# Kernel optimization log

Hardware: AMD Instinct MI355X
Metric: run time of the kernel (lower is better)

## Reference

```python
import jax, jax.numpy as jnp
import numpy as np

N = 100_000          # nodes
E = 1_600_000        # edges (avg degree 16)
IN_DIM = 128
POS_DIM = 16
CONTENT_DIM = IN_DIM - POS_DIM   # 112
H = 4                # num_heads
D = 32               # out_dim per head (H*D == IN_DIM -> identity residual)
D4 = D // 4          # pos feature dim per head


def setup_inputs() -> dict:
    key = jax.random.key(0)
    ks = jax.random.split(key, 10)
    feat = jax.random.normal(ks[0], (N, IN_DIM), jnp.float32)
    src = jax.random.randint(ks[1], (E,), 0, N, jnp.int32)
    dst = jax.random.randint(ks[2], (E,), 0, N, jnp.int32)
    # learned parameters (xavier-ish scale)
    Wc = jax.random.normal(ks[3], (H * D, CONTENT_DIM), jnp.float32) * (1.0 / np.sqrt(CONTENT_DIM))
    Wp = jax.random.normal(ks[4], (H * D4, POS_DIM), jnp.float32) * (1.0 / np.sqrt(POS_DIM))
    attn_src = jax.random.normal(ks[5], (1, H, D), jnp.float32) * 0.1
    attn_dst = jax.random.normal(ks[6], (1, H, D), jnp.float32) * 0.1
    pos_attn_src = jax.random.normal(ks[7], (1, H, D4), jnp.float32) * 0.1
    pos_attn_dst = jax.random.normal(ks[8], (1, H, D4), jnp.float32) * 0.1
    att_comb = jnp.full((H, 2), 0.5, jnp.float32)  # nn.init.constant_(0.5)
    return {"feat": feat, "src": src, "dst": dst, "Wc": Wc, "Wp": Wp,
            "attn_src": attn_src, "attn_dst": attn_dst,
            "pos_attn_src": pos_attn_src, "pos_attn_dst": pos_attn_dst,
            "att_comb": att_comb}


def reference(feat, src, dst, Wc, Wp, attn_src, attn_dst,
              pos_attn_src, pos_attn_dst, att_comb):
    content = feat[:, :-POS_DIM]                       # [N, CONTENT_DIM]
    pos = feat[:, -POS_DIM:]                           # [N, POS_DIM]
    hc = (content @ Wc.T).reshape(N, H, D)             # [N, H, D]
    hp = (pos @ Wp.T).reshape(N, H, D4)                # [N, H, D4]

    # per-node attention projections (reduce over feature dim once)
    es = jnp.einsum('nhd,hd->nh', hc, attn_src[0])     # [N, H]
    ed = jnp.einsum('nhd,hd->nh', hc, attn_dst[0])
    ps = jnp.einsum('nhd,hd->nh', hp, pos_attn_src[0])
    pd = jnp.einsum('nhd,hd->nh', hp, pos_attn_dst[0])

    # per-edge combined score + leaky relu (slope 0.2)
    content_e = es[src] + ed[dst]                      # [E, H]
    pos_e = ps[src] + pd[dst]
    e = content_e * att_comb[:, 0] + pos_e * att_comb[:, 1]
    e = jnp.where(e > 0, e, 0.2 * e)

    # edge softmax grouped by destination node
    emax = jax.ops.segment_max(e, dst, num_segments=N)     # [N, H]
    ex = jnp.exp(e - emax[dst])
    esum = jax.ops.segment_sum(ex, dst, num_segments=N)    # [N, H]
    a = ex / esum[dst]                                     # [E, H]

    # weighted message aggregation: ft[v] = sum_{(u,v)} a_uv * hc[u]
    ft = jax.ops.segment_sum(a[:, :, None] * hc[src], dst, num_segments=N)  # [N, H, D]

    h = ft.reshape(N, H * D) + feat   # identity residual (in_dim == out_dim*num_heads)
    diversity_loss = jnp.zeros((), jnp.float32)  # eval path
    return h, diversity_loss
```

## Files before the change

### kernel.cpp

```cpp
#include <hip/hip_runtime.h>
#include <hip/hip_bf16.h>

#define NN 100000
#define NE 1600000
#define FD 128
#define CD 112
#define PDIM 16
#define NH 4
#define NB_SCAN 391
#define NSHARD 8
#define SHARD 12500
#define NE4 400000
#define NB_E4 1563
#define NB_HIST (NSHARD * NB_E4)

#define NOUT 144
#define MBLK 64
#define NGB 1563

#define GRP 72
#define NGRP 196
#define FUSE_GRID (NGRP * GRP)

using bf16x8 = __attribute__((ext_vector_type(8))) short;
using f32x4  = __attribute__((ext_vector_type(4))) float;

__device__ __forceinline__ unsigned short f2bf(float x) {
    union { float f; unsigned int u; } v; v.f = x;
    return (unsigned short)((v.u + 0x7fffu + ((v.u >> 16) & 1u)) >> 16);
}
__device__ __forceinline__ float bf_lo(unsigned int u) { return __uint_as_float(u << 16); }
__device__ __forceinline__ float bf_hi(unsigned int u) { return __uint_as_float(u & 0xffff0000u); }

__device__ __forceinline__ bf16x8 pack8(const float4 g0, const float4 g1) {
    bf16x8 r;
    r[0] = (short)f2bf(g0.x); r[1] = (short)f2bf(g0.y);
    r[2] = (short)f2bf(g0.z); r[3] = (short)f2bf(g0.w);
    r[4] = (short)f2bf(g1.x); r[5] = (short)f2bf(g1.y);
    r[6] = (short)f2bf(g1.z); r[7] = (short)f2bf(g1.w);
    return r;
}

__global__ __launch_bounds__(256) void hist_prep_kernel(
    const int* __restrict__ dst, int* __restrict__ deg,
    const float* __restrict__ Wc, const float* __restrict__ Wp,
    const float* __restrict__ attn_src, const float* __restrict__ attn_dst,
    const float* __restrict__ pos_attn_src, const float* __restrict__ pos_attn_dst,
    const float* __restrict__ att_comb, unsigned short* __restrict__ wt)
{
    __shared__ float sA[NH * FD], sB[NH * FD];
    const int t = threadIdx.x;
    if (blockIdx.x < NB_HIST) {
        const int shard = blockIdx.x & (NSHARD - 1);
        const int i4 = (blockIdx.x >> 3) * 256 + t;
        if (i4 >= NE4) return;
        const int4 d4 = ((const int4*)dst)[i4];
        const int lo = shard * SHARD, hi = lo + SHARD;
        if (d4.x >= lo && d4.x < hi) atomicAdd(&deg[d4.x], 1);
        if (d4.y >= lo && d4.y < hi) atomicAdd(&deg[d4.y], 1);
        if (d4.z >= lo && d4.z < hi) atomicAdd(&deg[d4.z], 1);
        if (d4.w >= lo && d4.w < hi) atomicAdd(&deg[d4.w], 1);
        return;
    }
    #pragma unroll
    for (int r = 0; r < 2; ++r) {
        const int idx = t + r * 256;
        const int h = idx >> 7, k = idx & 127;
        const float c0 = att_comb[h * 2], c1 = att_comb[h * 2 + 1];
        float sa = 0.f, sb = 0.f;
        if (k < CD) {
            #pragma unroll 8
            for (int d = 0; d < 32; ++d) {
                const float wv = Wc[(size_t)(h * 32 + d) * CD + k];
                sa = fmaf(wv, attn_src[h * 32 + d], sa);
                sb = fmaf(wv, attn_dst[h * 32 + d], sb);
            }
            sa *= c0; sb *= c0;
        } else {
            const int k2 = k - CD;
            #pragma unroll
            for (int d4 = 0; d4 < 8; ++d4) {
                const float wv = Wp[(h * 8 + d4) * PDIM + k2];
                sa = fmaf(wv, pos_attn_src[h * 8 + d4], sa);
                sb = fmaf(wv, pos_attn_dst[h * 8 + d4], sb);
            }
            sa *= c1; sb *= c1;
        }
        sA[idx] = sa; sB[idx] = sb;
    }
    __syncthreads();
    #pragma unroll
    for (int it = 0; it < 72; ++it) {
        const int e = t + it * 256;
        const int row = e >> 7, k = e & 127;
        float val;
        if (row < 128)      val = (k < CD) ? Wc[(size_t)row * CD + k] : 0.f;
        else if (row < 132) val = sA[(row - 128) * FD + k];
        else if (row < 136) val = sB[(row - 132) * FD + k];
        else                val = 0.f;
        wt[e] = f2bf(val);
    }
}

__global__ __launch_bounds__(256) void scan1_kernel(const int* __restrict__ deg,
                                                    int* __restrict__ tmp,
                                                    int* __restrict__ bsum) {
    __shared__ int sh[256];
    const int t = threadIdx.x, b = blockIdx.x, i = b * 256 + t;
    const int v = (i < NN) ? deg[i] : 0;
    sh[t] = v;
    __syncthreads();
    #pragma unroll
    for (int off = 1; off < 256; off <<= 1) {
        const int x = (t >= off) ? sh[t - off] : 0;
        __syncthreads();
        sh[t] += x;
        __syncthreads();
    }
    if (i < NN) tmp[i] = sh[t] - v;
    if (t == 255) bsum[b] = sh[t];
}

__global__ __launch_bounds__(512) void scan2_kernel(int* __restrict__ bsum) {
    __shared__ int sh[512];
    const int t = threadIdx.x;
    const int v = (t < NB_SCAN) ? bsum[t] : 0;
    sh[t] = v;
    __syncthreads();
    #pragma unroll
    for (int off = 1; off < 512; off <<= 1) {
        const int x = (t >= off) ? sh[t - off] : 0;
        __syncthreads();
        sh[t] += x;
        __syncthreads();
    }
    if (t < NB_SCAN) bsum[t] = sh[t] - v;
}

__global__ __launch_bounds__(256) void scan3_kernel(const int* __restrict__ tmp,
                                                    const int* __restrict__ bsum,
                                                    int* __restrict__ row_ptr,
                                                    int* __restrict__ cursor) {
    const int i = blockIdx.x * 256 + threadIdx.x;
    if (i < NN) {
        const int v = tmp[i] + bsum[blockIdx.x];
        row_ptr[i] = v;
        cursor[i] = v;
    }
    if (i == 0) row_ptr[NN] = NE;
}

__global__ __launch_bounds__(256) void scatter_mfma_kernel(
    const int* __restrict__ src, const int* __restrict__ dst,
    int* __restrict__ cursor, int* __restrict__ col,
    const float* __restrict__ feat, const unsigned short* __restrict__ wt,
    unsigned short* __restrict__ hc_bf, float* __restrict__ A,
    float* __restrict__ B)
{
    const int bid = blockIdx.x;
    const int grp = bid / GRP, r = bid % GRP;
    const int t = threadIdx.x;

    if (r < 64) {
        const int sid = grp * 64 + r;
        const int shard = sid & (NSHARD - 1);
        const int i4 = (sid >> 3) * 256 + t;
        if (i4 >= NE4) return;
        const int4 d4 = ((const int4*)dst)[i4];
        const int4 s4 = ((const int4*)src)[i4];
        const int lo = shard * SHARD, hi = lo + SHARD;
        if (d4.x >= lo && d4.x < hi) col[atomicAdd(&cursor[d4.x], 1)] = s4.x;
        if (d4.y >= lo && d4.y < hi) col[atomicAdd(&cursor[d4.y], 1)] = s4.y;
        if (d4.z >= lo && d4.z < hi) col[atomicAdd(&cursor[d4.z], 1)] = s4.z;
        if (d4.w >= lo && d4.w < hi) col[atomicAdd(&cursor[d4.w], 1)] = s4.w;
        return;
    }

    const int g = grp * 8 + (r - 64);
    if (g >= NGB) return;
    const int n0 = g * MBLK;
    const int w = t >> 6;
    const int lane = t & 63;
    const int mr = lane & 15, quad = lane >> 4;
    const int node_row = n0 + w * 16 + mr;
    const size_t frow = (size_t)(node_row < NN ? node_row : 0) * FD;

    f32x4 acc[9];
    #pragma unroll
    for (int i = 0; i < 9; ++i) acc[i] = (f32x4){0.f, 0.f, 0.f, 0.f};

    #pragma unroll
    for (int kk = 0; kk < 4; ++kk) {
        const float4* fp = (const float4*)(feat + frow + kk * 32 + quad * 8);
        const bf16x8 a = pack8(fp[0], fp[1]);
        #pragma unroll
        for (int tt = 0; tt < 9; ++tt) {
            const bf16x8 b =
                *(const bf16x8*)&wt[(size_t)(tt * 16 + mr) * FD + kk * 32 + quad * 8];
            acc[tt] = __builtin_amdgcn_mfma_f32_16x16x32_bf16(a, b, acc[tt], 0, 0, 0);
        }
    }

    #pragma unroll
    for (int tt = 0; tt < 8; ++tt) {
        const int colc = tt * 16 + mr;
        #pragma unroll
        for (int rr = 0; rr < 4; ++rr) {
            const int node = n0 + w * 16 + quad * 4 + rr;
            if (node < NN) hc_bf[(size_t)node * FD + colc] = f2bf(acc[tt][rr]);
        }
    }
    #pragma unroll
    for (int rr = 0; rr < 4; ++rr) {
        const int node = n0 + w * 16 + quad * 4 + rr;
        if (node < NN) {
            if (mr < 4)      A[(size_t)node * NH + mr] = acc[8][rr];
            else if (mr < 8) B[(size_t)node * NH + (mr - 4)] = acc[8][rr];
        }
    }
}

__global__ __launch_bounds__(256) void agg_kernel(
    const int* __restrict__ row_ptr, const int* __restrict__ col,
    const float* __restrict__ A, const float* __restrict__ B,
    const uint2* __restrict__ hc_u2,
    const float* __restrict__ feat, float* __restrict__ out)
{
    const int n = blockIdx.x * 8 + (threadIdx.x >> 5);
    const int il = threadIdx.x & 31;
    const int hme = il >> 3;
    const int hbase = threadIdx.x & 0x20;
    const int gbase = hbase | (il & 0x18);
    const int r0 = row_ptr[n], r1 = row_ptr[n + 1];
    const float bh = B[(size_t)n * NH + hme];

    float ssum = 0.f;
    float acc0 = 0.f, acc1 = 0.f, acc2 = 0.f, acc3 = 0.f;

    int p = r0;
    while (p < r1) {
        const int cnt = (r1 - p < 32) ? (r1 - p) : 32;
        const int cidx = (il < cnt) ? col[p + il] : 0;
        for (int q = 0; q < cnt; q += 16) {
            const int j = il & 7;
            const int myc0 = __shfl(cidx, hbase | (q + j));
            const int myc1 = __shfl(cidx, hbase | (q + 8 + j));
            float w0 = 0.f, w1 = 0.f;
            if (q + j < cnt) {
                float e = A[(size_t)myc0 * NH + hme] + bh;
                e = e > 0.f ? e : 0.2f * e;
                w0 = __expf(e);
            }
            if (q + 8 + j < cnt) {
                float e = A[(size_t)myc1 * NH + hme] + bh;
                e = e > 0.f ? e : 0.2f * e;
                w1 = __expf(e);
            }
            int cm[16];
            #pragma unroll
            for (int m = 0; m < 16; ++m)
                cm[m] = __shfl(cidx, hbase | (q + m));
            uint2 u[16];
            #pragma unroll
            for (int m = 0; m < 16; ++m)
                u[m] = hc_u2[(size_t)cm[m] * 32 + il];
            #pragma unroll
            for (int m = 0; m < 16; ++m) {
                const float wm = (m < 8) ? __shfl(w0, gbase | m)
                                         : __shfl(w1, gbase | (m - 8));
                ssum += wm;
                acc0 = fmaf(wm, bf_lo(u[m].x), acc0);
                acc1 = fmaf(wm, bf_hi(u[m].x), acc1);
                acc2 = fmaf(wm, bf_lo(u[m].y), acc2);
                acc3 = fmaf(wm, bf_hi(u[m].y), acc3);
            }
        }
        p += cnt;
    }

    const float inv = ssum > 0.f ? 1.f / ssum : 0.f;
    const float4 fv = ((const float4*)(feat + (size_t)n * FD))[il];
    float4 ov;
    ov.x = acc0 * inv + fv.x;
    ov.y = acc1 * inv + fv.y;
    ov.z = acc2 * inv + fv.z;
    ov.w = acc3 * inv + fv.w;
    ((float4*)(out + (size_t)n * FD))[il] = ov;

    if (blockIdx.x == 0 && threadIdx.x == 0) out[(size_t)NN * FD] = 0.f;
}

extern "C" void kernel_launch(void* const* d_in, const int* in_sizes, int n_in,
                              void* d_out, int out_size, void* d_ws, size_t ws_size,
                              hipStream_t stream) {
    const float* feat         = (const float*)d_in[0];
    const int*   src          = (const int*)d_in[1];
    const int*   dst          = (const int*)d_in[2];
    const float* Wc           = (const float*)d_in[3];
    const float* Wp           = (const float*)d_in[4];
    const float* attn_src     = (const float*)d_in[5];
    const float* attn_dst     = (const float*)d_in[6];
    const float* pos_attn_src = (const float*)d_in[7];
    const float* pos_attn_dst = (const float*)d_in[8];
    const float* att_comb     = (const float*)d_in[9];
    float* out = (float*)d_out;

    char* w = (char*)d_ws;
    unsigned short* hc_bf = (unsigned short*)w;        w += (size_t)NN * FD * 2;
    float* A       = (float*)w;                        w += (size_t)NN * NH * 4;
    float* B       = (float*)w;                        w += (size_t)NN * NH * 4;
    int*   deg     = (int*)w;                          w += (size_t)NN * 4;
    int*   tmp     = (int*)w;                          w += (size_t)NN * 4;
    int*   row_ptr = (int*)w;                          w += (size_t)(NN + 4) * 4;
    int*   cursor  = (int*)w;                          w += (size_t)NN * 4;
    int*   bsum    = (int*)w;                          w += 512 * 4;
    unsigned short* wt = (unsigned short*)w;           w += (size_t)NOUT * FD * 2;
    int*   col     = (int*)w;

    hipMemsetAsync(deg, 0, (size_t)NN * sizeof(int), stream);
    hist_prep_kernel<<<NB_HIST + 1, 256, 0, stream>>>(dst, deg, Wc, Wp,
        attn_src, attn_dst, pos_attn_src, pos_attn_dst, att_comb, wt);
    scan1_kernel<<<NB_SCAN, 256, 0, stream>>>(deg, tmp, bsum);
    scan2_kernel<<<1, 512, 0, stream>>>(bsum);
    scan3_kernel<<<NB_SCAN, 256, 0, stream>>>(tmp, bsum, row_ptr, cursor);
    scatter_mfma_kernel<<<FUSE_GRID, 256, 0, stream>>>(src, dst, cursor, col,
        feat, wt, hc_bf, A, B);
    agg_kernel<<<NN / 8, 256, 0, stream>>>(row_ptr, col, A, B,
                                           (const uint2*)hc_bf, feat, out);
}
```

Measured before the change: 362.8 us.

## Record per-edge rank during histogram to make CSR scatter atomic-free

```diff
diff --git a/kernel.cpp b/kernel.cpp
--- a/kernel.cpp
+++ b/kernel.cpp
@@ -12,7 +12,6 @@
 #define SHARD 12500
 #define NE4 400000
 #define NB_E4 1563
-#define NB_HIST (NSHARD * NB_E4)
 
 #define NOUT 144
 #define MBLK 64
@@ -41,8 +40,7 @@
     return r;
 }
 
-__global__ __launch_bounds__(256) void hist_prep_kernel(
-    const int* __restrict__ dst, int* __restrict__ deg,
+__global__ __launch_bounds__(256) void prep_kernel(
     const float* __restrict__ Wc, const float* __restrict__ Wp,
     const float* __restrict__ attn_src, const float* __restrict__ attn_dst,
     const float* __restrict__ pos_attn_src, const float* __restrict__ pos_attn_dst,
@@ -50,18 +48,6 @@
 {
     __shared__ float sA[NH * FD], sB[NH * FD];
     const int t = threadIdx.x;
-    if (blockIdx.x < NB_HIST) {
-        const int shard = blockIdx.x & (NSHARD - 1);
-        const int i4 = (blockIdx.x >> 3) * 256 + t;
-        if (i4 >= NE4) return;
-        const int4 d4 = ((const int4*)dst)[i4];
-        const int lo = shard * SHARD, hi = lo + SHARD;
-        if (d4.x >= lo && d4.x < hi) atomicAdd(&deg[d4.x], 1);
-        if (d4.y >= lo && d4.y < hi) atomicAdd(&deg[d4.y], 1);
-        if (d4.z >= lo && d4.z < hi) atomicAdd(&deg[d4.z], 1);
-        if (d4.w >= lo && d4.w < hi) atomicAdd(&deg[d4.w], 1);
-        return;
-    }
     #pragma unroll
     for (int r = 0; r < 2; ++r) {
         const int idx = t + r * 256;
@@ -102,6 +88,76 @@
     }
 }
 
+__global__ __launch_bounds__(256) void hist_mfma_kernel(
+    const int* __restrict__ dst, int* __restrict__ deg,
+    unsigned char* __restrict__ rank_b,
+    const float* __restrict__ feat, const unsigned short* __restrict__ wt,
+    unsigned short* __restrict__ hc_bf, float* __restrict__ A,
+    float* __restrict__ B)
+{
+    const int bid = blockIdx.x;
+    const int grp = bid / GRP, r = bid % GRP;
+    const int t = threadIdx.x;
+
+    if (r < 64) {
+        const int sid = grp * 64 + r;
+        const int shard = sid & (NSHARD - 1);
+        const int i4 = (sid >> 3) * 256 + t;
+        if (i4 >= NE4) return;
+        const int4 d4 = ((const int4*)dst)[i4];
+        const int lo = shard * SHARD, hi = lo + SHARD;
+        const int e0 = i4 * 4;
+        if (d4.x >= lo && d4.x < hi) rank_b[e0 + 0] = (unsigned char)atomicAdd(&deg[d4.x], 1);
+        if (d4.y >= lo && d4.y < hi) rank_b[e0 + 1] = (unsigned char)atomicAdd(&deg[d4.y], 1);
+        if (d4.z >= lo && d4.z < hi) rank_b[e0 + 2] = (unsigned char)atomicAdd(&deg[d4.z], 1);
+        if (d4.w >= lo && d4.w < hi) rank_b[e0 + 3] = (unsigned char)atomicAdd(&deg[d4.w], 1);
+        return;
+    }
+
+    const int g = grp * 8 + (r - 64);
+    if (g >= NGB) return;
+    const int n0 = g * MBLK;
+    const int w = t >> 6;
+    const int lane = t & 63;
+    const int mr = lane & 15, quad = lane >> 4;
+    const int node_row = n0 + w * 16 + mr;
+    const size_t frow = (size_t)(node_row < NN ? node_row : 0) * FD;
+
+    f32x4 acc[9];
+    #pragma unroll
+    for (int i = 0; i < 9; ++i) acc[i] = (f32x4){0.f, 0.f, 0.f, 0.f};
+
+    #pragma unroll
+    for (int kk = 0; kk < 4; ++kk) {
+        const float4* fp = (const float4*)(feat + frow + kk * 32 + quad * 8);
+        const bf16x8 a = pack8(fp[0], fp[1]);
+        #pragma unroll
+        for (int tt = 0; tt < 9; ++tt) {
+            const bf16x8 b =
+                *(const bf16x8*)&wt[(size_t)(tt * 16 + mr) * FD + kk * 32 + quad * 8];
+            acc[tt] = __builtin_amdgcn_mfma_f32_16x16x32_bf16(a, b, acc[tt], 0, 0, 0);
+        }
+    }
+
+    #pragma unroll
+    for (int tt = 0; tt < 8; ++tt) {
+        const int colc = tt * 16 + mr;
+        #pragma unroll
+        for (int rr = 0; rr < 4; ++rr) {
+            const int node = n0 + w * 16 + quad * 4 + rr;
+            if (node < NN) hc_bf[(size_t)node * FD + colc] = f2bf(acc[tt][rr]);
+        }
+    }
+    #pragma unroll
+    for (int rr = 0; rr < 4; ++rr) {
+        const int node = n0 + w * 16 + quad * 4 + rr;
+        if (node < NN) {
+            if (mr < 4)      A[(size_t)node * NH + mr] = acc[8][rr];
+            else if (mr < 8) B[(size_t)node * NH + (mr - 4)] = acc[8][rr];
+        }
+    }
+}
+
 __global__ __launch_bounds__(256) void scan1_kernel(const int* __restrict__ deg,
                                                     int* __restrict__ tmp,
                                                     int* __restrict__ bsum) {
@@ -139,85 +195,26 @@
 
 __global__ __launch_bounds__(256) void scan3_kernel(const int* __restrict__ tmp,
                                                     const int* __restrict__ bsum,
-                                                    int* __restrict__ row_ptr,
-                                                    int* __restrict__ cursor) {
+                                                    int* __restrict__ row_ptr) {
     const int i = blockIdx.x * 256 + threadIdx.x;
-    if (i < NN) {
-        const int v = tmp[i] + bsum[blockIdx.x];
-        row_ptr[i] = v;
-        cursor[i] = v;
-    }
+    if (i < NN) row_ptr[i] = tmp[i] + bsum[blockIdx.x];
     if (i == 0) row_ptr[NN] = NE;
 }
 
-__global__ __launch_bounds__(256) void scatter_mfma_kernel(
+__global__ __launch_bounds__(256) void scatter_kernel(
     const int* __restrict__ src, const int* __restrict__ dst,
-    int* __restrict__ cursor, int* __restrict__ col,
-    const float* __restrict__ feat, const unsigned short* __restrict__ wt,
-    unsigned short* __restrict__ hc_bf, float* __restrict__ A,
-    float* __restrict__ B)
+    const unsigned char* __restrict__ rank_b, const int* __restrict__ row_ptr,
+    int* __restrict__ col)
 {
-    const int bid = blockIdx.x;
-    const int grp = bid / GRP, r = bid % GRP;
-    const int t = threadIdx.x;
-
-    if (r < 64) {
-        const int sid = grp * 64 + r;
-        const int shard = sid & (NSHARD - 1);
-        const int i4 = (sid >> 3) * 256 + t;
-        if (i4 >= NE4) return;
-        const int4 d4 = ((const int4*)dst)[i4];
-        const int4 s4 = ((const int4*)src)[i4];
-        const int lo = shard * SHARD, hi = lo + SHARD;
-        if (d4.x >= lo && d4.x < hi) col[atomicAdd(&cursor[d4.x], 1)] = s4.x;
-        if (d4.y >= lo && d4.y < hi) col[atomicAdd(&cursor[d4.y], 1)] = s4.y;
-        if (d4.z >= lo && d4.z < hi) col[atomicAdd(&cursor[d4.z], 1)] = s4.z;
-        if (d4.w >= lo && d4.w < hi) col[atomicAdd(&cursor[d4.w], 1)] = s4.w;
-        return;
-    }
-
-    const int g = grp * 8 + (r - 64);
-    if (g >= NGB) return;
-    const int n0 = g * MBLK;
-    const int w = t >> 6;
-    const int lane = t & 63;
-    const int mr = lane & 15, quad = lane >> 4;
-    const int node_row = n0 + w * 16 + mr;
-    const size_t frow = (size_t)(node_row < NN ? node_row : 0) * FD;
-
-    f32x4 acc[9];
-    #pragma unroll
-    for (int i = 0; i < 9; ++i) acc[i] = (f32x4){0.f, 0.f, 0.f, 0.f};
-
-    #pragma unroll
-    for (int kk = 0; kk < 4; ++kk) {
-        const float4* fp = (const float4*)(feat + frow + kk * 32 + quad * 8);
-        const bf16x8 a = pack8(fp[0], fp[1]);
-        #pragma unroll
-        for (int tt = 0; tt < 9; ++tt) {
-            const bf16x8 b =
-                *(const bf16x8*)&wt[(size_t)(tt * 16 + mr) * FD + kk * 32 + quad * 8];
-            acc[tt] = __builtin_amdgcn_mfma_f32_16x16x32_bf16(a, b, acc[tt], 0, 0, 0);
-        }
-    }
-
-    #pragma unroll
-    for (int tt = 0; tt < 8; ++tt) {
-        const int colc = tt * 16 + mr;
-        #pragma unroll
-        for (int rr = 0; rr < 4; ++rr) {
-            const int node = n0 + w * 16 + quad * 4 + rr;
-            if (node < NN) hc_bf[(size_t)node * FD + colc] = f2bf(acc[tt][rr]);
-        }
-    }
-    #pragma unroll
-    for (int rr = 0; rr < 4; ++rr) {
-        const int node = n0 + w * 16 + quad * 4 + rr;
-        if (node < NN) {
-            if (mr < 4)      A[(size_t)node * NH + mr] = acc[8][rr];
-            else if (mr < 8) B[(size_t)node * NH + (mr - 4)] = acc[8][rr];
-        }
-    }
+    const int i4 = blockIdx.x * 256 + threadIdx.x;
+    if (i4 >= NE4) return;
+    const int4 d4 = ((const int4*)dst)[i4];
+    const int4 s4 = ((const int4*)src)[i4];
+    const unsigned int r4 = ((const unsigned int*)rank_b)[i4];
+    col[row_ptr[d4.x] + (int)(r4 & 0xffu)]         = s4.x;
+    col[row_ptr[d4.y] + (int)((r4 >> 8) & 0xffu)]  = s4.y;
+    col[row_ptr[d4.z] + (int)((r4 >> 16) & 0xffu)] = s4.z;
+    col[row_ptr[d4.w] + (int)(r4 >> 24)]           = s4.w;
 }
 
 __global__ __launch_bounds__(256) void agg_kernel(
@@ -312,19 +309,20 @@
     int*   deg     = (int*)w;                          w += (size_t)NN * 4;
     int*   tmp     = (int*)w;                          w += (size_t)NN * 4;
     int*   row_ptr = (int*)w;                          w += (size_t)(NN + 4) * 4;
-    int*   cursor  = (int*)w;                          w += (size_t)NN * 4;
     int*   bsum    = (int*)w;                          w += 512 * 4;
     unsigned short* wt = (unsigned short*)w;           w += (size_t)NOUT * FD * 2;
-    int*   col     = (int*)w;
+    int*   col     = (int*)w;                          w += (size_t)NE * 4;
+    unsigned char* rank_b = (unsigned char*)w;
 
     hipMemsetAsync(deg, 0, (size_t)NN * sizeof(int), stream);
-    hist_prep_kernel<<<NB_HIST + 1, 256, 0, stream>>>(dst, deg, Wc, Wp,
-        attn_src, attn_dst, pos_attn_src, pos_attn_dst, att_comb, wt);
+    prep_kernel<<<1, 256, 0, stream>>>(Wc, Wp, attn_src, attn_dst,
+                                       pos_attn_src, pos_attn_dst, att_comb, wt);
+    hist_mfma_kernel<<<FUSE_GRID, 256, 0, stream>>>(dst, deg, rank_b,
+                                                    feat, wt, hc_bf, A, B);
     scan1_kernel<<<NB_SCAN, 256, 0, stream>>>(deg, tmp, bsum);
     scan2_kernel<<<1, 512, 0, stream>>>(bsum);
-    scan3_kernel<<<NB_SCAN, 256, 0, stream>>>(tmp, bsum, row_ptr, cursor);
-    scatter_mfma_kernel<<<FUSE_GRID, 256, 0, stream>>>(src, dst, cursor, col,
-        feat, wt, hc_bf, A, B);
+    scan3_kernel<<<NB_SCAN, 256, 0, stream>>>(tmp, bsum, row_ptr);
+    scatter_kernel<<<NB_E4, 256, 0, stream>>>(src, dst, rank_b, row_ptr, col);
     agg_kernel<<<NN / 8, 256, 0, stream>>>(row_ptr, col, A, B,
                                            (const uint2*)hc_bf, feat, out);
 }
```

After: 331.3 us. 1.09x faster.
